# Performance work log

Hardware: AMD Instinct MI355X
Metric: run time of the kernel (lower is better)

Reference implementation:

```python
import jax, jax.numpy as jnp
import numpy as np


def setup_inputs() -> dict:
    key = jax.random.key(0)
    kq, kk, kv = jax.random.split(key, 3)
    B, QH, KH, S, D = 2, 32, 8, 2048, 128
    Q = jax.random.normal(kq, (B, QH, S, D), dtype=jnp.float32)
    K = jax.random.normal(kk, (B, KH, S, D), dtype=jnp.float32)
    V = jax.random.normal(kv, (B, KH, S, D), dtype=jnp.float32)
    return {"Q": Q, "K": K, "V": V}


def reference(Q, K, V):
    B, QH, S, D = Q.shape
    KH = K.shape[1]
    G = QH // KH  # group size: query heads per KV head
    scale = jnp.sqrt(jnp.asarray(D, dtype=Q.dtype))
    # Group query heads: [B, KH, G, S, D]
    Qg = Q.reshape(B, KH, G, S, D)
    # scores: [B, KH, G, S, S]
    scores = jnp.einsum('bkgsd,bktd->bkgst', Qg, K) / scale
    probs = jax.nn.softmax(scores, axis=-1)
    out = jnp.einsum('bkgst,bktd->bkgsd', probs, V)
    return out.reshape(B, QH, S, D)
```

## Files before the change

kernel.cpp:

```cpp
#include <hip/hip_runtime.h>

typedef unsigned short u16;
typedef unsigned int u32;
typedef u16 u16x4 __attribute__((ext_vector_type(4)));
typedef u16 u16x8 __attribute__((ext_vector_type(8)));
typedef u32 u32x4 __attribute__((ext_vector_type(4)));
typedef __bf16 bf16x8 __attribute__((ext_vector_type(8)));
typedef float f32x4 __attribute__((ext_vector_type(4)));

#define NB   2
#define NQH  32
#define NKH  8
#define SEQ  2048
#define DIM  128
#define QT   128
#define NT   32
#define HALFU16 4096
#define TILEU16 8192
#define HEADU16 (NT * TILEU16)
#define VOFFU16 (16 * HEADU16)

__device__ __forceinline__ u16 f2bf(float f) {
  u32 u = __builtin_bit_cast(u32, f);
  u += 0x7FFFu + ((u >> 16) & 1u);
  return (u16)(u >> 16);
}
__device__ __forceinline__ u32 cvtpk(float lo, float hi) {
  u32 r;
  asm("v_cvt_pk_bf16_f32 %0, %1, %2" : "=v"(r) : "v"(lo), "v"(hi));
  return r;
}
__device__ __forceinline__ f32x4 mfma16(u16x8 a, u16x8 b, f32x4 c) {
  return __builtin_amdgcn_mfma_f32_16x16x32_bf16(
      __builtin_bit_cast(bf16x8, a), __builtin_bit_cast(bf16x8, b), c, 0, 0, 0);
}
__device__ __forceinline__ void gl_lds16(const u16* g, u16* l) {
  __builtin_amdgcn_global_load_lds(
      (const __attribute__((address_space(1))) u32*)(const void*)g,
      (__attribute__((address_space(3))) u32*)(void*)l, 16, 0, 0);
}

__global__ __launch_bounds__(256) void prep(const float* __restrict__ Kg,
                                            const float* __restrict__ Vg,
                                            u16* __restrict__ ws) {
  const int bid = blockIdx.x;
  const int tid = threadIdx.x;
  const int tile = bid & 511;
  const size_t sbase = (size_t)(tile >> 5) * SEQ * DIM + (size_t)(tile & 31) * 64 * DIM;
  if (bid < 512) {
    const float* src = Kg + sbase;
    u16* img = ws + (size_t)tile * TILEU16;
    #pragma unroll
    for (int u = 0; u < 8; ++u) {
      int c = tid + 256 * u;
      int j = c >> 5;
      int dm = (c & 31) * 4;
      float4 v = *(const float4*)(src + j * DIM + dm);
      u16x4 w = { f2bf(v.x), f2bf(v.y), f2bf(v.z), f2bf(v.w) };
      *(u16x4*)(img + j * 128 + (dm ^ ((j & 7) << 3))) = w;
    }
  } else {
    const float* src = Vg + sbase;
    u16* img = ws + VOFFU16 + (size_t)tile * TILEU16;
    #pragma unroll
    for (int u = 0; u < 4; ++u) {
      int g = tid + 256 * u;
      int half = g >> 9;
      int gg = g & 511;
      int d = gg >> 2;
      int grp = gg & 3;
      int gr = grp ^ ((d >> 1) & 3);
      u16x8 w;
      #pragma unroll
      for (int i = 0; i < 8; ++i) {
        int key = 16 * (i >> 2) + 4 * gr + (i & 3);
        w[i] = f2bf(src[(32 * half + key) * DIM + d]);
      }
      *(u16x8*)(img + half * HALFU16 + d * 32 + grp * 8) = w;
    }
  }
}

__global__ __launch_bounds__(256) void gqa_fwd(const float* __restrict__ Qg,
                                               const u16* __restrict__ ws,
                                               float* __restrict__ Og) {
  __shared__ __align__(16) u16 sK[2][TILEU16];
  __shared__ __align__(16) u16 sV[TILEU16];

  const int tid  = threadIdx.x;
  const int lane = tid & 63;
  const int wave = tid >> 6;
  const int lr   = lane & 15;
  const int lg   = lane >> 4;

  const int id = blockIdx.x;
  const int wg = (id & 7) * 128 + (id >> 3);
  const int qtile = wg & 15;
  const int bqh   = wg >> 4;
  const int b     = bqh >> 5;
  const int qh    = bqh & 31;
  const int kh    = qh >> 2;

  const size_t qbase = (size_t)bqh * SEQ * DIM;
  const u16* imgK = ws + (size_t)(b * NKH + kh) * HEADU16;
  const u16* imgV = imgK + VOFFU16;
  const int qrow_w = qtile * QT + wave * 32;

  auto issueK = [&](int t, int pb) {
    const u16* g = imgK + (size_t)t * TILEU16;
    #pragma unroll
    for (int u = 0; u < 4; ++u) {
      const int q = u * 4 + wave;
      gl_lds16(g + q * 512 + lane * 8, &sK[pb][q * 512]);
    }
  };
  auto issueV = [&](int t) {
    const u16* g = imgV + (size_t)t * TILEU16;
    #pragma unroll
    for (int u = 0; u < 4; ++u) {
      const int q = u * 4 + wave;
      gl_lds16(g + q * 512 + lane * 8, &sV[q * 512]);
    }
  };
  issueK(0, 0);

  const float s2 = 0.08838834764831845f * 1.4426950408889634f;

  u16x8 qf0[4], qf1[4];
  #pragma unroll
  for (int s = 0; s < 4; ++s) {
    const float* qp0 = Qg + qbase + (size_t)(qrow_w + lr) * DIM + 32 * s + 8 * lg;
    float4 a = *(const float4*)qp0;
    float4 c = *(const float4*)(qp0 + 4);
    qf0[s] = __builtin_bit_cast(u16x8, u32x4{
        cvtpk(a.x * s2, a.y * s2), cvtpk(a.z * s2, a.w * s2),
        cvtpk(c.x * s2, c.y * s2), cvtpk(c.z * s2, c.w * s2) });
    const float* qp1 = qp0 + 16 * DIM;
    float4 e = *(const float4*)qp1;
    float4 f = *(const float4*)(qp1 + 4);
    qf1[s] = __builtin_bit_cast(u16x8, u32x4{
        cvtpk(e.x * s2, e.y * s2), cvtpk(e.z * s2, e.w * s2),
        cvtpk(f.x * s2, f.y * s2), cvtpk(f.z * s2, f.w * s2) });
  }

  const f32x4 zero4 = {0.f, 0.f, 0.f, 0.f};
  f32x4 o0[8], o1[8];
  #pragma unroll
  for (int dt = 0; dt < 8; ++dt) { o0[dt] = zero4; o1[dt] = zero4; }
  float lsum0 = 0.f, lsum1 = 0.f;

  const int swzK = (lr & 7) << 3;
  const int swzV = (lg ^ ((lr >> 1) & 3)) << 3;

  auto qk_exp = [&](int pb, int g, u32* pk0, u32* pk1) {
    f32x4 s0 = zero4, s1 = zero4;
    __builtin_amdgcn_s_setprio(1);
    #pragma unroll
    for (int s = 0; s < 4; ++s) {
      u16x8 kf = *(const u16x8*)&sK[pb][(g * 16 + lr) * 128 + ((32 * s + 8 * lg) ^ swzK)];
      s0 = mfma16(kf, qf0[s], s0);
      s1 = mfma16(kf, qf1[s], s1);
    }
    __builtin_amdgcn_s_setprio(0);
    float a0 = exp2f(s0[0]), b0 = exp2f(s0[1]);
    float c0 = exp2f(s0[2]), d0 = exp2f(s0[3]);
    lsum0 += (a0 + b0) + (c0 + d0);
    pk0[0] = cvtpk(a0, b0); pk0[1] = cvtpk(c0, d0);
    float a1 = exp2f(s1[0]), b1 = exp2f(s1[1]);
    float c1 = exp2f(s1[2]), d1 = exp2f(s1[3]);
    lsum1 += (a1 + b1) + (c1 + d1);
    pk1[0] = cvtpk(a1, b1); pk1[1] = cvtpk(c1, d1);
  };
  auto pv_half = [&](int half, const u32* pk0, const u32* pk1) {
    u16x8 af0 = __builtin_bit_cast(u16x8, u32x4{pk0[0], pk0[1], pk0[2], pk0[3]});
    u16x8 af1 = __builtin_bit_cast(u16x8, u32x4{pk1[0], pk1[1], pk1[2], pk1[3]});
    __builtin_amdgcn_s_setprio(1);
    #pragma unroll
    for (int dt = 0; dt < 8; ++dt) {
      u16x8 vf = *(const u16x8*)&sV[half * HALFU16 + (16 * dt + lr) * 32 + swzV];
      o0[dt] = mfma16(af0, vf, o0[dt]);
      o1[dt] = mfma16(af1, vf, o1[dt]);
    }
    __builtin_amdgcn_s_setprio(0);
  };

  #pragma unroll 1
  for (int T = 0; T < NT; ++T) {
    const int pb = T & 1;
    __builtin_amdgcn_s_barrier();
    issueV(T);
    issueK((T + 1) & (NT - 1), pb ^ 1);
    asm volatile("s_waitcnt vmcnt(8)" ::: "memory");
    __builtin_amdgcn_s_barrier();

    u32 pkA0[4], pkA1[4];
    qk_exp(pb, 0, &pkA0[0], &pkA1[0]);
    qk_exp(pb, 1, &pkA0[2], &pkA1[2]);
    asm volatile("s_waitcnt vmcnt(4)" ::: "memory");
    __builtin_amdgcn_s_barrier();
    pv_half(0, pkA0, pkA1);

    u32 pkB0[4], pkB1[4];
    qk_exp(pb, 2, &pkB0[0], &pkB1[0]);
    qk_exp(pb, 3, &pkB0[2], &pkB1[2]);
    pv_half(1, pkB0, pkB1);
  }
  asm volatile("s_waitcnt vmcnt(0)" ::: "memory");

  float r0 = lsum0;
  r0 += __shfl_xor(r0, 16, 64); r0 += __shfl_xor(r0, 32, 64);
  float r1 = lsum1;
  r1 += __shfl_xor(r1, 16, 64); r1 += __shfl_xor(r1, 32, 64);
  float li0 = 1.0f / r0, li1 = 1.0f / r1;
  #pragma unroll
  for (int e = 0; e < 4; ++e) {
    float lo0 = __shfl(li0, 4 * lg + e, 64);
    float lo1 = __shfl(li1, 4 * lg + e, 64);
    float* op0 = Og + qbase + (size_t)(qrow_w + 4 * lg + e) * DIM;
    float* op1 = op0 + 16 * DIM;
    #pragma unroll
    for (int dt = 0; dt < 8; ++dt) {
      op0[dt * 16 + lr] = o0[dt][e] * lo0;
      op1[dt * 16 + lr] = o1[dt][e] * lo1;
    }
  }
}

extern "C" void kernel_launch(void* const* d_in, const int* in_sizes, int n_in,
                              void* d_out, int out_size, void* d_ws, size_t ws_size,
                              hipStream_t stream) {
  const float* Q = (const float*)d_in[0];
  const float* K = (const float*)d_in[1];
  const float* V = (const float*)d_in[2];
  float* O = (float*)d_out;
  u16* ws = (u16*)d_ws;
  prep<<<dim3(1024), 256, 0, stream>>>(K, V, ws);
  gqa_fwd<<<dim3((SEQ / QT) * NB * NQH), 256, 0, stream>>>(Q, ws, O);
}
```

Baseline: 180.3 us.

## Read V fragments directly from global memory and prefetch K two tiles ahead

Removes the shared-memory V staging buffer. Each wave now loads its V fragments straight from the pre-swizzled global image, and the PV MFMA is transposed so every lane holds a full output row. K tiles are double-buffered with a two-tile lookahead, leaving one barrier per iteration. The epilogue writes float4 rows and no longer needs lane shuffles. The exchange is fewer LDS writes and barriers for more global and L2 traffic, since each wave re-reads V, and exposed global latency on the V loads inside the MFMA chain.

```diff
diff --git a/kernel.cpp b/kernel.cpp
--- a/kernel.cpp
+++ b/kernel.cpp
@@ -85,7 +85,6 @@
                                                const u16* __restrict__ ws,
                                                float* __restrict__ Og) {
   __shared__ __align__(16) u16 sK[2][TILEU16];
-  __shared__ __align__(16) u16 sV[TILEU16];
 
   const int tid  = threadIdx.x;
   const int lane = tid & 63;
@@ -114,15 +113,8 @@
       gl_lds16(g + q * 512 + lane * 8, &sK[pb][q * 512]);
     }
   };
-  auto issueV = [&](int t) {
-    const u16* g = imgV + (size_t)t * TILEU16;
-    #pragma unroll
-    for (int u = 0; u < 4; ++u) {
-      const int q = u * 4 + wave;
-      gl_lds16(g + q * 512 + lane * 8, &sV[q * 512]);
-    }
-  };
   issueK(0, 0);
+  issueK(1, 1);
 
   const float s2 = 0.08838834764831845f * 1.4426950408889634f;
 
@@ -150,60 +142,51 @@
   float lsum0 = 0.f, lsum1 = 0.f;
 
   const int swzK = (lr & 7) << 3;
-  const int swzV = (lg ^ ((lr >> 1) & 3)) << 3;
-
-  auto qk_exp = [&](int pb, int g, u32* pk0, u32* pk1) {
-    f32x4 s0 = zero4, s1 = zero4;
-    __builtin_amdgcn_s_setprio(1);
-    #pragma unroll
-    for (int s = 0; s < 4; ++s) {
-      u16x8 kf = *(const u16x8*)&sK[pb][(g * 16 + lr) * 128 + ((32 * s + 8 * lg) ^ swzK)];
-      s0 = mfma16(kf, qf0[s], s0);
-      s1 = mfma16(kf, qf1[s], s1);
-    }
-    __builtin_amdgcn_s_setprio(0);
-    float a0 = exp2f(s0[0]), b0 = exp2f(s0[1]);
-    float c0 = exp2f(s0[2]), d0 = exp2f(s0[3]);
-    lsum0 += (a0 + b0) + (c0 + d0);
-    pk0[0] = cvtpk(a0, b0); pk0[1] = cvtpk(c0, d0);
-    float a1 = exp2f(s1[0]), b1 = exp2f(s1[1]);
-    float c1 = exp2f(s1[2]), d1 = exp2f(s1[3]);
-    lsum1 += (a1 + b1) + (c1 + d1);
-    pk1[0] = cvtpk(a1, b1); pk1[1] = cvtpk(c1, d1);
-  };
-  auto pv_half = [&](int half, const u32* pk0, const u32* pk1) {
-    u16x8 af0 = __builtin_bit_cast(u16x8, u32x4{pk0[0], pk0[1], pk0[2], pk0[3]});
-    u16x8 af1 = __builtin_bit_cast(u16x8, u32x4{pk1[0], pk1[1], pk1[2], pk1[3]});
-    __builtin_amdgcn_s_setprio(1);
-    #pragma unroll
-    for (int dt = 0; dt < 8; ++dt) {
-      u16x8 vf = *(const u16x8*)&sV[half * HALFU16 + (16 * dt + lr) * 32 + swzV];
-      o0[dt] = mfma16(af0, vf, o0[dt]);
-      o1[dt] = mfma16(af1, vf, o1[dt]);
-    }
-    __builtin_amdgcn_s_setprio(0);
-  };
+  const int grp  = lg ^ ((lr >> 1) & 3);
+  const u16* vlane = imgV + lr * 32 + grp * 8;
+
+  __syncthreads();
 
   #pragma unroll 1
   for (int T = 0; T < NT; ++T) {
     const int pb = T & 1;
+    #pragma unroll
+    for (int h = 0; h < 2; ++h) {
+      u32 pk0[4], pk1[4];
+      #pragma unroll
+      for (int g2 = 0; g2 < 2; ++g2) {
+        const int g = 2 * h + g2;
+        f32x4 s0 = zero4, s1 = zero4;
+        #pragma unroll
+        for (int s = 0; s < 4; ++s) {
+          u16x8 kf = *(const u16x8*)&sK[pb][(g * 16 + lr) * 128 + ((32 * s + 8 * lg) ^ swzK)];
+          s0 = mfma16(kf, qf0[s], s0);
+          s1 = mfma16(kf, qf1[s], s1);
+        }
+        float a0 = exp2f(s0[0]), b0 = exp2f(s0[1]);
+        float c0 = exp2f(s0[2]), d0 = exp2f(s0[3]);
+        lsum0 += (a0 + b0) + (c0 + d0);
+        pk0[2 * g2]     = cvtpk(a0, b0);
+        pk0[2 * g2 + 1] = cvtpk(c0, d0);
+        float a1 = exp2f(s1[0]), b1 = exp2f(s1[1]);
+        float c1 = exp2f(s1[2]), d1 = exp2f(s1[3]);
+        lsum1 += (a1 + b1) + (c1 + d1);
+        pk1[2 * g2]     = cvtpk(a1, b1);
+        pk1[2 * g2 + 1] = cvtpk(c1, d1);
+      }
+      u16x8 af0 = __builtin_bit_cast(u16x8, u32x4{pk0[0], pk0[1], pk0[2], pk0[3]});
+      u16x8 af1 = __builtin_bit_cast(u16x8, u32x4{pk1[0], pk1[1], pk1[2], pk1[3]});
+      const u16* vtile = vlane + (size_t)T * TILEU16 + h * HALFU16;
+      #pragma unroll
+      for (int dt = 0; dt < 8; ++dt) {
+        u16x8 vf = *(const u16x8*)(vtile + dt * 512);
+        o0[dt] = mfma16(vf, af0, o0[dt]);
+        o1[dt] = mfma16(vf, af1, o1[dt]);
+      }
+    }
+    asm volatile("s_waitcnt vmcnt(0)" ::: "memory");
     __builtin_amdgcn_s_barrier();
-    issueV(T);
-    issueK((T + 1) & (NT - 1), pb ^ 1);
-    asm volatile("s_waitcnt vmcnt(8)" ::: "memory");
-    __builtin_amdgcn_s_barrier();
-
-    u32 pkA0[4], pkA1[4];
-    qk_exp(pb, 0, &pkA0[0], &pkA1[0]);
-    qk_exp(pb, 1, &pkA0[2], &pkA1[2]);
-    asm volatile("s_waitcnt vmcnt(4)" ::: "memory");
-    __builtin_amdgcn_s_barrier();
-    pv_half(0, pkA0, pkA1);
-
-    u32 pkB0[4], pkB1[4];
-    qk_exp(pb, 2, &pkB0[0], &pkB1[0]);
-    qk_exp(pb, 3, &pkB0[2], &pkB1[2]);
-    pv_half(1, pkB0, pkB1);
+    issueK((T + 2) & (NT - 1), pb);
   }
   asm volatile("s_waitcnt vmcnt(0)" ::: "memory");
 
@@ -211,18 +194,15 @@
   r0 += __shfl_xor(r0, 16, 64); r0 += __shfl_xor(r0, 32, 64);
   float r1 = lsum1;
   r1 += __shfl_xor(r1, 16, 64); r1 += __shfl_xor(r1, 32, 64);
-  float li0 = 1.0f / r0, li1 = 1.0f / r1;
+  const float li0 = 1.0f / r0, li1 = 1.0f / r1;
+  float* op0 = Og + qbase + (size_t)(qrow_w + lr) * DIM;
+  float* op1 = op0 + 16 * DIM;
   #pragma unroll
-  for (int e = 0; e < 4; ++e) {
-    float lo0 = __shfl(li0, 4 * lg + e, 64);
-    float lo1 = __shfl(li1, 4 * lg + e, 64);
-    float* op0 = Og + qbase + (size_t)(qrow_w + 4 * lg + e) * DIM;
-    float* op1 = op0 + 16 * DIM;
-    #pragma unroll
-    for (int dt = 0; dt < 8; ++dt) {
-      op0[dt * 16 + lr] = o0[dt][e] * lo0;
-      op1[dt * 16 + lr] = o1[dt][e] * lo1;
-    }
+  for (int dt = 0; dt < 8; ++dt) {
+    f32x4 w0 = o0[dt] * li0;
+    f32x4 w1 = o1[dt] * li1;
+    *(float4*)(op0 + 16 * dt + 4 * lg) = __builtin_bit_cast(float4, w0);
+    *(float4*)(op1 + 16 * dt + 4 * lg) = __builtin_bit_cast(float4, w1);
   }
 }
 
```

New measurement: 386.0 us. 114% more time.
